# Kernel optimization log

Measured on AMD Instinct MI355X. Metric: run time of the kernel, lower is better.

## Reference

```python
import jax, jax.numpy as jnp
import numpy as np

INPUT_DIM = 1024
HIDDEN_DIM = 1024


def setup_inputs() -> dict:
    key = jax.random.key(0)
    ks = jax.random.split(key, 7)
    s = 1.0 / np.sqrt(INPUT_DIM)
    x = jax.random.normal(ks[0], (4, 2048, INPUT_DIM), dtype=jnp.float32)
    Wq = jax.random.uniform(ks[1], (INPUT_DIM, HIDDEN_DIM), minval=-s, maxval=s, dtype=jnp.float32)
    bq = jax.random.uniform(ks[2], (HIDDEN_DIM,), minval=-s, maxval=s, dtype=jnp.float32)
    Wk = jax.random.uniform(ks[3], (INPUT_DIM, HIDDEN_DIM), minval=-s, maxval=s, dtype=jnp.float32)
    bk = jax.random.uniform(ks[4], (HIDDEN_DIM,), minval=-s, maxval=s, dtype=jnp.float32)
    Wv = jax.random.uniform(ks[5], (INPUT_DIM, HIDDEN_DIM), minval=-s, maxval=s, dtype=jnp.float32)
    bv = jax.random.uniform(ks[6], (HIDDEN_DIM,), minval=-s, maxval=s, dtype=jnp.float32)
    return {"x": x, "Wq": Wq, "bq": bq, "Wk": Wk, "bk": bk, "Wv": Wv, "bv": bv}


def reference(x, Wq, bq, Wk, bk, Wv, bv):
    # Q, K, V: [B, S, H]
    Q = jnp.einsum('bsd,dh->bsh', x, Wq) + bq
    K = jnp.einsum('bsd,dh->bsh', x, Wk) + bk
    V = jnp.einsum('bsd,dh->bsh', x, Wv) + bv
    scale = 1.0 / jnp.sqrt(jnp.array(Q.shape[-1], dtype=Q.dtype))
    scores = jnp.einsum('bqh,bkh->bqk', Q, K) * scale  # [B, S, S]
    attn = jax.nn.softmax(scores, axis=-1)
    return jnp.einsum('bqk,bkh->bqh', attn, V)
```

## Files before the change

### kernel.cpp

```cpp
#include <hip/hip_runtime.h>
#include <hip/hip_bf16.h>
#include <stdint.h>

typedef unsigned short u16;
typedef __attribute__((ext_vector_type(8))) short short8;
typedef __attribute__((ext_vector_type(4))) float floatx4;

#define BATCH 4
#define SEQ   2048
#define DIM   1024

__device__ inline u16 f2bf(float f) {
  union { float f; uint32_t u; } v; v.f = f;
  uint32_t r = v.u + 0x7fffu + ((v.u >> 16) & 1u);
  return (u16)(r >> 16);
}

__device__ inline uint32_t f2bf2(float lo, float hi) {
  __hip_bfloat162 h = __float22bfloat162_rn(float2{lo, hi});
  union { __hip_bfloat162 h; uint32_t u; } v; v.h = h;
  return v.u;
}

__device__ inline void gload_lds16(const u16* g, u16* l) {
  __builtin_amdgcn_global_load_lds((const __attribute__((address_space(1))) uint32_t*)g,
                                   (__attribute__((address_space(3))) uint32_t*)l,
                                   16, 0, 0);
}

__global__ __launch_bounds__(256) void prep(const float* __restrict__ x,
                                            const float* __restrict__ Wq,
                                            const float* __restrict__ Wk,
                                            const float* __restrict__ Wv,
                                            const float* __restrict__ bq,
                                            const float* __restrict__ bk,
                                            const float* __restrict__ bv,
                                            u16* __restrict__ Xb,
                                            u16* __restrict__ Wt,
                                            float* __restrict__ bias,
                                            float* __restrict__ lsum) {
  __shared__ u16 tile[32][33];
  const int bx = blockIdx.x;
  if (bx < 8192) {
    size_t i = ((size_t)bx * 256 + threadIdx.x) * 4;
    float4 v = *(const float4*)(x + i);
    uint2 o;
    o.x = f2bf2(v.x, v.y);
    o.y = f2bf2(v.z, v.w);
    *(uint2*)(Xb + i) = o;
    if (bx < 8) {
      float4 z = {0.f, 0.f, 0.f, 0.f};
      *(float4*)(lsum + (size_t)bx * 1024 + threadIdx.x * 4) = z;
    }
    return;
  }
  const int t = bx - 8192;
  const int tz = t >> 10;
  const int bxx = t & 31;
  const int byy = (t >> 5) & 31;
  const float* W = (tz == 0) ? Wq : (tz == 1) ? Wk : Wv;
  u16* o = Wt + (size_t)tz * (1u << 20);
  if (bxx == 0 && byy == 0) {
    const float* bsrc = (tz == 0) ? bq : (tz == 1) ? bk : bv;
    float4 b4 = *(const float4*)(bsrc + threadIdx.x * 4);
    *(float4*)(bias + tz * 1024 + threadIdx.x * 4) = b4;
  }
  int c0 = bxx * 32, r0 = byy * 32;
  int tx = threadIdx.x & 31, ty = threadIdx.x >> 5;
#pragma unroll
  for (int p = 0; p < 4; ++p)
    tile[p * 8 + ty][tx] = f2bf(W[(size_t)(r0 + p * 8 + ty) * DIM + c0 + tx]);
  __syncthreads();
#pragma unroll
  for (int p = 0; p < 4; ++p)
    o[(size_t)(c0 + p * 8 + ty) * DIM + r0 + tx] = tile[tx][p * 8 + ty];
}


__global__ __launch_bounds__(256, 4)
void qkv_fused(const u16* __restrict__ Xb, const u16* __restrict__ Wt,
               u16* __restrict__ Q, u16* __restrict__ Vt,
               const float* __restrict__ bias) {
  constexpr int K = 1024;
  __shared__ u16 ldsA[128 * 64];
  __shared__ u16 ldsB[128 * 64];
  const int lane = threadIdx.x & 63;
  const int wave = threadIdx.x >> 6;
  const int z = blockIdx.z;

  int mt, nt, N;
  const u16 *Ab, *Bb;
  if (z < 2) {
    mt = blockIdx.x; nt = blockIdx.y; N = 1024;
    Ab = Xb + (size_t)mt * 128 * K;
    Bb = Wt + (size_t)z * (1u << 20) + (size_t)nt * 128 * K;
  } else {
    nt = blockIdx.x; mt = blockIdx.y; N = 8192;
    Ab = Wt + (size_t)2 * (1u << 20) + (size_t)mt * 128 * K;
    Bb = Xb + (size_t)nt * 128 * K;
  }

  const int sr = lane >> 2;
  const int sc = ((lane & 3) ^ ((lane >> 3) & 3)) * 8;
  const u16* gA0 = Ab + (size_t)(wave * 32 + sr) * K + sc;
  const u16* gB0 = Bb + (size_t)(wave * 32 + sr) * K + sc;
  u16* lA0 = ldsA + wave * 1024;
  u16* lB0 = ldsB + wave * 1024;
  constexpr int SL = 4096;

  const int wm = (wave >> 1) * 64;
  const int wn = (wave & 1) * 64;
  const int fr = lane & 15;
  const int fk = ((lane >> 4) ^ ((fr >> 1) & 3)) * 8;
  const u16* la = ldsA + (wm + fr) * 32 + fk;
  const u16* lb = ldsB + (wn + fr) * 32 + fk;

  floatx4 acc[4][4] = {};

  for (int kt = 0; kt < K; kt += 64) {
    __syncthreads();
#pragma unroll
    for (int i = 0; i < 2; ++i) {
      gload_lds16(gA0 + kt + (size_t)(16 * i) * K, lA0 + i * 512);
      gload_lds16(gA0 + kt + 32 + (size_t)(16 * i) * K, lA0 + SL + i * 512);
      gload_lds16(gB0 + kt + (size_t)(16 * i) * K, lB0 + i * 512);
      gload_lds16(gB0 + kt + 32 + (size_t)(16 * i) * K, lB0 + SL + i * 512);
    }
    __syncthreads();
#pragma unroll
    for (int ks = 0; ks < 2; ++ks) {
      short8 a[4], b[4];
#pragma unroll
      for (int i = 0; i < 4; ++i) a[i] = *(const short8*)(la + ks * SL + i * 512);
#pragma unroll
      for (int i = 0; i < 4; ++i) b[i] = *(const short8*)(lb + ks * SL + i * 512);
#pragma unroll
      for (int mi = 0; mi < 4; ++mi)
#pragma unroll
        for (int ni = 0; ni < 4; ++ni)
          acc[mi][ni] = __builtin_amdgcn_mfma_f32_16x16x32_bf16(a[mi], b[ni], acc[mi][ni], 0, 0, 0);
    }
  }

  const int er = (lane >> 4) * 4;
  const int ec = lane & 15;
  const int r0 = mt * 128 + wm;
  const int c0 = nt * 128 + wn;

  if (z < 2) {
    u16* C = Q + (size_t)z * (8u << 20);
    const float* bz = bias + z * 1024;
    const float zs = (z == 0) ? 0.03125f : 1.0f;
#pragma unroll
    for (int mi = 0; mi < 4; ++mi)
#pragma unroll
      for (int ni = 0; ni < 4; ++ni) {
        const int col = c0 + ni * 16 + ec;
        const float bb = bz[col];
        const int row = r0 + mi * 16 + er;
        const uint32_t p0 = f2bf2((acc[mi][ni][0] + bb) * zs, (acc[mi][ni][1] + bb) * zs);
        const uint32_t p1 = f2bf2((acc[mi][ni][2] + bb) * zs, (acc[mi][ni][3] + bb) * zs);
        C[(size_t)(row + 0) * N + col] = (u16)p0;
        C[(size_t)(row + 1) * N + col] = (u16)(p0 >> 16);
        C[(size_t)(row + 2) * N + col] = (u16)p1;
        C[(size_t)(row + 3) * N + col] = (u16)(p1 >> 16);
      }
  } else {
    const float* bz = bias + 2 * 1024;
#pragma unroll
    for (int mi = 0; mi < 4; ++mi) {
      float bb[4];
#pragma unroll
      for (int r = 0; r < 4; ++r) bb[r] = bz[r0 + mi * 16 + er + r];
#pragma unroll
      for (int ni = 0; ni < 4; ++ni) {
        const int col = c0 + ni * 16 + ec;
        const size_t base = (size_t)(col >> 11) * (1u << 21) + (col & 2047);
        const int row = r0 + mi * 16 + er;
        const uint32_t p0 = f2bf2(acc[mi][ni][0] + bb[0], acc[mi][ni][1] + bb[1]);
        const uint32_t p1 = f2bf2(acc[mi][ni][2] + bb[2], acc[mi][ni][3] + bb[3]);
        Vt[base + (size_t)(row + 0) * 2048] = (u16)p0;
        Vt[base + (size_t)(row + 1) * 2048] = (u16)(p0 >> 16);
        Vt[base + (size_t)(row + 2) * 2048] = (u16)p1;
        Vt[base + (size_t)(row + 3) * 2048] = (u16)(p1 >> 16);
      }
    }
  }
}

template <int EPI, int SWIZ, int TM>
__global__ __launch_bounds__(256, (TM == 256) ? 2 : 4)
void gemm_bt(const u16* __restrict__ A, const u16* __restrict__ Bt,
             void* __restrict__ Cv, float* __restrict__ lsum,
             int M, int N, int K, size_t sA, size_t sB, size_t sC) {
  constexpr int MI = TM / 32;
  constexpr int AS = TM / 64;
  __shared__ u16 ldsA[TM * 64];
  __shared__ u16 ldsB[128 * 64];
  const int lane = threadIdx.x & 63;
  const int wave = threadIdx.x >> 6;

  int mt, nt;
  if (SWIZ == 2) {
    const int lin = blockIdx.x;
    const int c = lin & 7, j = lin >> 3;
    mt = 4 * (c >> 1) + (j & 3);
    nt = 4 * (c & 1) + (j >> 2);
  } else {
    const int lin = blockIdx.x;
    const int c = lin & 7, j = lin >> 3;
    mt = 4 * (c & 1) + (j & 3);
    nt = 4 * (c >> 1) + (j >> 2);
  }

  const u16* Ab = A + sA * blockIdx.z + (size_t)mt * TM * K;
  const u16* Bb = Bt + sB * blockIdx.z + (size_t)nt * 128 * K;

  const int sr = lane >> 2;
  const int sc = ((lane & 3) ^ ((lane >> 3) & 3)) * 8;
  const u16* gA0 = Ab + (size_t)(wave * (TM / 4) + sr) * K + sc;
  const u16* gB0 = Bb + (size_t)(wave * 32 + sr) * K + sc;
  u16* lA0 = ldsA + wave * (TM / 4) * 32;
  u16* lB0 = ldsB + wave * 1024;
  constexpr int SLA = TM * 32;
  constexpr int SLB = 4096;

  const int wm = (wave >> 1) * (TM / 2);
  const int wn = (wave & 1) * 64;
  const int fr = lane & 15;
  const int fk = ((lane >> 4) ^ ((fr >> 1) & 3)) * 8;
  const u16* la = ldsA + (wm + fr) * 32 + fk;
  const u16* lb = ldsB + (wn + fr) * 32 + fk;

  floatx4 acc[MI][4] = {};

  for (int kt = 0; kt < K; kt += 64) {
    __syncthreads();
#pragma unroll
    for (int i = 0; i < AS; ++i) {
      gload_lds16(gA0 + kt + (size_t)(16 * i) * K, lA0 + i * 512);
      gload_lds16(gA0 + kt + 32 + (size_t)(16 * i) * K, lA0 + SLA + i * 512);
    }
#pragma unroll
    for (int i = 0; i < 2; ++i) {
      gload_lds16(gB0 + kt + (size_t)(16 * i) * K, lB0 + i * 512);
      gload_lds16(gB0 + kt + 32 + (size_t)(16 * i) * K, lB0 + SLB + i * 512);
    }
    __syncthreads();
#pragma unroll
    for (int ks = 0; ks < 2; ++ks) {
      short8 a[MI], b[4];
#pragma unroll
      for (int i = 0; i < MI; ++i)
        a[i] = *(const short8*)(la + ks * SLA + i * 512);
#pragma unroll
      for (int i = 0; i < 4; ++i)
        b[i] = *(const short8*)(lb + ks * SLB + i * 512);
#pragma unroll
      for (int mi = 0; mi < MI; ++mi)
#pragma unroll
        for (int ni = 0; ni < 4; ++ni)
          acc[mi][ni] = __builtin_amdgcn_mfma_f32_16x16x32_bf16(a[mi], b[ni], acc[mi][ni], 0, 0, 0);
    }
  }

  const int er = (lane >> 4) * 4;
  const int ec = lane & 15;
  const int r0 = mt * TM + wm;
  const int c0 = nt * 128 + wn;

  if (EPI == 1) {
    u16* C = (u16*)Cv + sC * blockIdx.z;
    float* lz = lsum + blockIdx.z * 2048;
#pragma unroll
    for (int mi = 0; mi < MI; ++mi) {
      float rs[4] = {0.f, 0.f, 0.f, 0.f};
#pragma unroll
      for (int ni = 0; ni < 4; ++ni) {
        const int col = c0 + ni * 16 + ec;
        const int row = r0 + mi * 16 + er;
        float e[4];
#pragma unroll
        for (int r = 0; r < 4; ++r) {
          e[r] = exp2f(acc[mi][ni][r] * 1.44269504088896340736f);
          rs[r] += e[r];
        }
        const uint32_t p0 = f2bf2(e[0], e[1]);
        const uint32_t p1 = f2bf2(e[2], e[3]);
        C[(size_t)(row + 0) * N + col] = (u16)p0;
        C[(size_t)(row + 1) * N + col] = (u16)(p0 >> 16);
        C[(size_t)(row + 2) * N + col] = (u16)p1;
        C[(size_t)(row + 3) * N + col] = (u16)(p1 >> 16);
      }
#pragma unroll
      for (int o = 1; o < 16; o <<= 1)
#pragma unroll
        for (int r = 0; r < 4; ++r) rs[r] += __shfl_xor(rs[r], o);
      if ((lane & 15) == 0) {
#pragma unroll
        for (int r = 0; r < 4; ++r)
          atomicAdd(&lz[r0 + mi * 16 + er + r], rs[r]);
      }
    }
  } else {
    float* C = (float*)Cv + sC * blockIdx.z;
    const float* lz = lsum + blockIdx.z * 2048;
#pragma unroll
    for (int mi = 0; mi < MI; ++mi) {
      float inv[4];
#pragma unroll
      for (int r = 0; r < 4; ++r) inv[r] = 1.0f / lz[r0 + mi * 16 + er + r];
#pragma unroll
      for (int ni = 0; ni < 4; ++ni) {
        const int col = c0 + ni * 16 + ec;
#pragma unroll
        for (int r = 0; r < 4; ++r) {
          const int row = r0 + mi * 16 + er + r;
          C[(size_t)row * N + col] = acc[mi][ni][r] * inv[r];
        }
      }
    }
  }
}

extern "C" void kernel_launch(void* const* d_in, const int* in_sizes, int n_in,
                              void* d_out, int out_size, void* d_ws, size_t ws_size,
                              hipStream_t stream) {
  const float* x  = (const float*)d_in[0];
  const float* Wq = (const float*)d_in[1];
  const float* bq = (const float*)d_in[2];
  const float* Wk = (const float*)d_in[3];
  const float* bk = (const float*)d_in[4];
  const float* Wv = (const float*)d_in[5];
  const float* bv = (const float*)d_in[6];
  float* out = (float*)d_out;

  char* ws = (char*)d_ws;
  const size_t MB = 1ull << 20;
  u16* Q    = (u16*)(ws + 0 * MB);
  u16* Kb   = (u16*)(ws + 16 * MB);
  u16* Vt   = (u16*)(ws + 48 * MB);
  u16* Xb   = (u16*)(ws + 64 * MB);
  u16* Wt   = (u16*)(ws + 80 * MB);
  float* bias = (float*)(ws + 86 * MB);
  float* lsum = (float*)(ws + 87 * MB);
  u16* P    = (u16*)(ws + 88 * MB);
  (void)Kb; (void)ws_size; (void)in_sizes; (void)n_in; (void)out_size;

  prep<<<11264, 256, 0, stream>>>(x, Wq, Wk, Wv, bq, bk, bv, Xb, Wt, bias, lsum);
  qkv_fused<<<dim3(64, 8, 3), 256, 0, stream>>>(Xb, Wt, Q, Vt, bias);
  gemm_bt<1, 4, 256><<<dim3(128, 1, 4), 256, 0, stream>>>(
      Q, Kb, P, lsum, 2048, 2048, 1024,
      (size_t)2097152, (size_t)2097152, (size_t)4194304);
  gemm_bt<2, 2, 128><<<dim3(128, 1, 4), 256, 0, stream>>>(
      P, Vt, out, lsum, 2048, 1024, 2048,
      (size_t)4194304, (size_t)2097152, (size_t)2097152);
}
```

Before: 232.7 us.

## Split PV GEMM over K with atomic accumulation and shrink score tiles

The PV GEMM is split into two halves along the key dimension, doubling its grid to 256 blocks per batch, and partial results are accumulated into the output with float atomicAdd. The output is zeroed by extra blocks in the prep kernel. The score GEMM moves from 256-row to 128-row tiles, also doubling its grid, and a shared k-loop helper replaces the templated GEMM. The aim is better CU occupancy on the MI355X's many CUs, at the cost of atomic traffic to the output and an extra zeroing pass.

```diff
diff --git a/kernel.cpp b/kernel.cpp
--- a/kernel.cpp
+++ b/kernel.cpp
@@ -38,7 +38,8 @@
                                             u16* __restrict__ Xb,
                                             u16* __restrict__ Wt,
                                             float* __restrict__ bias,
-                                            float* __restrict__ lsum) {
+                                            float* __restrict__ lsum,
+                                            float* __restrict__ out) {
   __shared__ u16 tile[32][33];
   const int bx = blockIdx.x;
   if (bx < 8192) {
@@ -54,6 +55,14 @@
     }
     return;
   }
+  if (bx >= 11264) {
+    const int b2 = bx - 11264;
+    const float4 z = {0.f, 0.f, 0.f, 0.f};
+#pragma unroll
+    for (int k = 0; k < 4; ++k)
+      *(float4*)(out + ((size_t)b2 * 1024 + k * 256 + threadIdx.x) * 4) = z;
+    return;
+  }
   const int t = bx - 8192;
   const int tz = t >> 10;
   const int bxx = t & 31;
@@ -77,11 +86,63 @@
 }
 
 
+template <int TM, int LD, int KLEN>
+__device__ __forceinline__ void kloop(const u16* __restrict__ Ab, const u16* __restrict__ Bb,
+                                      u16* __restrict__ ldsA, u16* __restrict__ ldsB,
+                                      int lane, int wave, floatx4 (&acc)[TM / 32][4]) {
+  constexpr int MI = TM / 32;
+  constexpr int AS = TM / 64;
+  const int sr = lane >> 2;
+  const int sc = ((lane & 3) ^ ((lane >> 3) & 3)) * 8;
+  const u16* gA0 = Ab + (size_t)(wave * (TM / 4) + sr) * LD + sc;
+  const u16* gB0 = Bb + (size_t)(wave * 32 + sr) * LD + sc;
+  u16* lA0 = ldsA + wave * (TM / 4) * 32;
+  u16* lB0 = ldsB + wave * 1024;
+  constexpr int SLA = TM * 32;
+  constexpr int SLB = 4096;
+
+  const int wm = (wave >> 1) * (TM / 2);
+  const int wn = (wave & 1) * 64;
+  const int fr = lane & 15;
+  const int fk = ((lane >> 4) ^ ((fr >> 1) & 3)) * 8;
+  const u16* la = ldsA + (wm + fr) * 32 + fk;
+  const u16* lb = ldsB + (wn + fr) * 32 + fk;
+
+  for (int kt = 0; kt < KLEN; kt += 64) {
+    __syncthreads();
+#pragma unroll
+    for (int i = 0; i < AS; ++i) {
+      gload_lds16(gA0 + kt + (size_t)(16 * i) * LD, lA0 + i * 512);
+      gload_lds16(gA0 + kt + 32 + (size_t)(16 * i) * LD, lA0 + SLA + i * 512);
+    }
+#pragma unroll
+    for (int i = 0; i < 2; ++i) {
+      gload_lds16(gB0 + kt + (size_t)(16 * i) * LD, lB0 + i * 512);
+      gload_lds16(gB0 + kt + 32 + (size_t)(16 * i) * LD, lB0 + SLB + i * 512);
+    }
+    __syncthreads();
+#pragma unroll
+    for (int ks = 0; ks < 2; ++ks) {
+      short8 a[MI], b[4];
+#pragma unroll
+      for (int i = 0; i < MI; ++i)
+        a[i] = *(const short8*)(la + ks * SLA + i * 512);
+#pragma unroll
+      for (int i = 0; i < 4; ++i)
+        b[i] = *(const short8*)(lb + ks * SLB + i * 512);
+#pragma unroll
+      for (int mi = 0; mi < MI; ++mi)
+#pragma unroll
+        for (int ni = 0; ni < 4; ++ni)
+          acc[mi][ni] = __builtin_amdgcn_mfma_f32_16x16x32_bf16(a[mi], b[ni], acc[mi][ni], 0, 0, 0);
+    }
+  }
+}
+
 __global__ __launch_bounds__(256, 4)
 void qkv_fused(const u16* __restrict__ Xb, const u16* __restrict__ Wt,
                u16* __restrict__ Q, u16* __restrict__ Vt,
                const float* __restrict__ bias) {
-  constexpr int K = 1024;
   __shared__ u16 ldsA[128 * 64];
   __shared__ u16 ldsB[128 * 64];
   const int lane = threadIdx.x & 63;
@@ -92,56 +153,19 @@
   const u16 *Ab, *Bb;
   if (z < 2) {
     mt = blockIdx.x; nt = blockIdx.y; N = 1024;
-    Ab = Xb + (size_t)mt * 128 * K;
-    Bb = Wt + (size_t)z * (1u << 20) + (size_t)nt * 128 * K;
+    Ab = Xb + (size_t)mt * 128 * 1024;
+    Bb = Wt + (size_t)z * (1u << 20) + (size_t)nt * 128 * 1024;
   } else {
     nt = blockIdx.x; mt = blockIdx.y; N = 8192;
-    Ab = Wt + (size_t)2 * (1u << 20) + (size_t)mt * 128 * K;
-    Bb = Xb + (size_t)nt * 128 * K;
-  }
-
-  const int sr = lane >> 2;
-  const int sc = ((lane & 3) ^ ((lane >> 3) & 3)) * 8;
-  const u16* gA0 = Ab + (size_t)(wave * 32 + sr) * K + sc;
-  const u16* gB0 = Bb + (size_t)(wave * 32 + sr) * K + sc;
-  u16* lA0 = ldsA + wave * 1024;
-  u16* lB0 = ldsB + wave * 1024;
-  constexpr int SL = 4096;
+    Ab = Wt + (size_t)2 * (1u << 20) + (size_t)mt * 128 * 1024;
+    Bb = Xb + (size_t)nt * 128 * 1024;
+  }
+
+  floatx4 acc[4][4] = {};
+  kloop<128, 1024, 1024>(Ab, Bb, ldsA, ldsB, lane, wave, acc);
 
   const int wm = (wave >> 1) * 64;
   const int wn = (wave & 1) * 64;
-  const int fr = lane & 15;
-  const int fk = ((lane >> 4) ^ ((fr >> 1) & 3)) * 8;
-  const u16* la = ldsA + (wm + fr) * 32 + fk;
-  const u16* lb = ldsB + (wn + fr) * 32 + fk;
-
-  floatx4 acc[4][4] = {};
-
-  for (int kt = 0; kt < K; kt += 64) {
-    __syncthreads();
-#pragma unroll
-    for (int i = 0; i < 2; ++i) {
-      gload_lds16(gA0 + kt + (size_t)(16 * i) * K, lA0 + i * 512);
-      gload_lds16(gA0 + kt + 32 + (size_t)(16 * i) * K, lA0 + SL + i * 512);
-      gload_lds16(gB0 + kt + (size_t)(16 * i) * K, lB0 + i * 512);
-      gload_lds16(gB0 + kt + 32 + (size_t)(16 * i) * K, lB0 + SL + i * 512);
-    }
-    __syncthreads();
-#pragma unroll
-    for (int ks = 0; ks < 2; ++ks) {
-      short8 a[4], b[4];
-#pragma unroll
-      for (int i = 0; i < 4; ++i) a[i] = *(const short8*)(la + ks * SL + i * 512);
-#pragma unroll
-      for (int i = 0; i < 4; ++i) b[i] = *(const short8*)(lb + ks * SL + i * 512);
-#pragma unroll
-      for (int mi = 0; mi < 4; ++mi)
-#pragma unroll
-        for (int ni = 0; ni < 4; ++ni)
-          acc[mi][ni] = __builtin_amdgcn_mfma_f32_16x16x32_bf16(a[mi], b[ni], acc[mi][ni], 0, 0, 0);
-    }
-  }
-
   const int er = (lane >> 4) * 4;
   const int ec = lane & 15;
   const int r0 = mt * 128 + wm;
@@ -188,136 +212,100 @@
   }
 }
 
-template <int EPI, int SWIZ, int TM>
-__global__ __launch_bounds__(256, (TM == 256) ? 2 : 4)
-void gemm_bt(const u16* __restrict__ A, const u16* __restrict__ Bt,
-             void* __restrict__ Cv, float* __restrict__ lsum,
-             int M, int N, int K, size_t sA, size_t sB, size_t sC) {
-  constexpr int MI = TM / 32;
-  constexpr int AS = TM / 64;
-  __shared__ u16 ldsA[TM * 64];
+__global__ __launch_bounds__(256, 4)
+void score_k(const u16* __restrict__ Q, u16* __restrict__ P, float* __restrict__ lsum) {
+  __shared__ u16 ldsA[128 * 64];
   __shared__ u16 ldsB[128 * 64];
   const int lane = threadIdx.x & 63;
   const int wave = threadIdx.x >> 6;
-
-  int mt, nt;
-  if (SWIZ == 2) {
-    const int lin = blockIdx.x;
-    const int c = lin & 7, j = lin >> 3;
-    mt = 4 * (c >> 1) + (j & 3);
-    nt = 4 * (c & 1) + (j >> 2);
-  } else {
-    const int lin = blockIdx.x;
-    const int c = lin & 7, j = lin >> 3;
-    mt = 4 * (c & 1) + (j & 3);
-    nt = 4 * (c >> 1) + (j >> 2);
-  }
-
-  const u16* Ab = A + sA * blockIdx.z + (size_t)mt * TM * K;
-  const u16* Bb = Bt + sB * blockIdx.z + (size_t)nt * 128 * K;
-
-  const int sr = lane >> 2;
-  const int sc = ((lane & 3) ^ ((lane >> 3) & 3)) * 8;
-  const u16* gA0 = Ab + (size_t)(wave * (TM / 4) + sr) * K + sc;
-  const u16* gB0 = Bb + (size_t)(wave * 32 + sr) * K + sc;
-  u16* lA0 = ldsA + wave * (TM / 4) * 32;
-  u16* lB0 = ldsB + wave * 1024;
-  constexpr int SLA = TM * 32;
-  constexpr int SLB = 4096;
-
-  const int wm = (wave >> 1) * (TM / 2);
+  const int z = blockIdx.z;
+  const int c = blockIdx.x & 7, j = blockIdx.x >> 3;
+  const int mt = 4 * (c >> 1) + (j & 3);
+  const int nt = 8 * (c & 1) + (j >> 2);
+  const u16* Ab = Q + (size_t)z * 2097152 + (size_t)mt * 128 * 1024;
+  const u16* Bb = Q + 8388608 + (size_t)z * 2097152 + (size_t)nt * 128 * 1024;
+
+  floatx4 acc[4][4] = {};
+  kloop<128, 1024, 1024>(Ab, Bb, ldsA, ldsB, lane, wave, acc);
+
+  const int wm = (wave >> 1) * 64;
   const int wn = (wave & 1) * 64;
-  const int fr = lane & 15;
-  const int fk = ((lane >> 4) ^ ((fr >> 1) & 3)) * 8;
-  const u16* la = ldsA + (wm + fr) * 32 + fk;
-  const u16* lb = ldsB + (wn + fr) * 32 + fk;
-
-  floatx4 acc[MI][4] = {};
-
-  for (int kt = 0; kt < K; kt += 64) {
-    __syncthreads();
-#pragma unroll
-    for (int i = 0; i < AS; ++i) {
-      gload_lds16(gA0 + kt + (size_t)(16 * i) * K, lA0 + i * 512);
-      gload_lds16(gA0 + kt + 32 + (size_t)(16 * i) * K, lA0 + SLA + i * 512);
-    }
-#pragma unroll
-    for (int i = 0; i < 2; ++i) {
-      gload_lds16(gB0 + kt + (size_t)(16 * i) * K, lB0 + i * 512);
-      gload_lds16(gB0 + kt + 32 + (size_t)(16 * i) * K, lB0 + SLB + i * 512);
-    }
-    __syncthreads();
-#pragma unroll
-    for (int ks = 0; ks < 2; ++ks) {
-      short8 a[MI], b[4];
-#pragma unroll
-      for (int i = 0; i < MI; ++i)
-        a[i] = *(const short8*)(la + ks * SLA + i * 512);
-#pragma unroll
-      for (int i = 0; i < 4; ++i)
-        b[i] = *(const short8*)(lb + ks * SLB + i * 512);
-#pragma unroll
-      for (int mi = 0; mi < MI; ++mi)
-#pragma unroll
-        for (int ni = 0; ni < 4; ++ni)
-          acc[mi][ni] = __builtin_amdgcn_mfma_f32_16x16x32_bf16(a[mi], b[ni], acc[mi][ni], 0, 0, 0);
-    }
-  }
-
   const int er = (lane >> 4) * 4;
   const int ec = lane & 15;
-  const int r0 = mt * TM + wm;
+  const int r0 = mt * 128 + wm;
   const int c0 = nt * 128 + wn;
-
-  if (EPI == 1) {
-    u16* C = (u16*)Cv + sC * blockIdx.z;
-    float* lz = lsum + blockIdx.z * 2048;
-#pragma unroll
-    for (int mi = 0; mi < MI; ++mi) {
-      float rs[4] = {0.f, 0.f, 0.f, 0.f};
-#pragma unroll
-      for (int ni = 0; ni < 4; ++ni) {
-        const int col = c0 + ni * 16 + ec;
-        const int row = r0 + mi * 16 + er;
-        float e[4];
-#pragma unroll
-        for (int r = 0; r < 4; ++r) {
-          e[r] = exp2f(acc[mi][ni][r] * 1.44269504088896340736f);
-          rs[r] += e[r];
-        }
-        const uint32_t p0 = f2bf2(e[0], e[1]);
-        const uint32_t p1 = f2bf2(e[2], e[3]);
-        C[(size_t)(row + 0) * N + col] = (u16)p0;
-        C[(size_t)(row + 1) * N + col] = (u16)(p0 >> 16);
-        C[(size_t)(row + 2) * N + col] = (u16)p1;
-        C[(size_t)(row + 3) * N + col] = (u16)(p1 >> 16);
+  u16* C = P + (size_t)z * 4194304;
+  float* lz = lsum + z * 2048;
+#pragma unroll
+  for (int mi = 0; mi < 4; ++mi) {
+    float rs[4] = {0.f, 0.f, 0.f, 0.f};
+#pragma unroll
+    for (int ni = 0; ni < 4; ++ni) {
+      const int col = c0 + ni * 16 + ec;
+      const int row = r0 + mi * 16 + er;
+      float e[4];
+#pragma unroll
+      for (int r = 0; r < 4; ++r) {
+        e[r] = exp2f(acc[mi][ni][r] * 1.44269504088896340736f);
+        rs[r] += e[r];
       }
-#pragma unroll
-      for (int o = 1; o < 16; o <<= 1)
-#pragma unroll
-        for (int r = 0; r < 4; ++r) rs[r] += __shfl_xor(rs[r], o);
-      if ((lane & 15) == 0) {
-#pragma unroll
-        for (int r = 0; r < 4; ++r)
-          atomicAdd(&lz[r0 + mi * 16 + er + r], rs[r]);
-      }
-    }
-  } else {
-    float* C = (float*)Cv + sC * blockIdx.z;
-    const float* lz = lsum + blockIdx.z * 2048;
-#pragma unroll
-    for (int mi = 0; mi < MI; ++mi) {
-      float inv[4];
-#pragma unroll
-      for (int r = 0; r < 4; ++r) inv[r] = 1.0f / lz[r0 + mi * 16 + er + r];
-#pragma unroll
-      for (int ni = 0; ni < 4; ++ni) {
-        const int col = c0 + ni * 16 + ec;
-#pragma unroll
-        for (int r = 0; r < 4; ++r) {
-          const int row = r0 + mi * 16 + er + r;
-          C[(size_t)row * N + col] = acc[mi][ni][r] * inv[r];
-        }
+      const uint32_t p0 = f2bf2(e[0], e[1]);
+      const uint32_t p1 = f2bf2(e[2], e[3]);
+      C[(size_t)(row + 0) * 2048 + col] = (u16)p0;
+      C[(size_t)(row + 1) * 2048 + col] = (u16)(p0 >> 16);
+      C[(size_t)(row + 2) * 2048 + col] = (u16)p1;
+      C[(size_t)(row + 3) * 2048 + col] = (u16)(p1 >> 16);
+    }
+#pragma unroll
+    for (int o = 1; o < 16; o <<= 1)
+#pragma unroll
+      for (int r = 0; r < 4; ++r) rs[r] += __shfl_xor(rs[r], o);
+    if ((lane & 15) == 0) {
+#pragma unroll
+      for (int r = 0; r < 4; ++r)
+        atomicAdd(&lz[r0 + mi * 16 + er + r], rs[r]);
+    }
+  }
+}
+
+__global__ __launch_bounds__(256, 4)
+void pv_k(const u16* __restrict__ P, const u16* __restrict__ Vt,
+          float* __restrict__ out, const float* __restrict__ lsum) {
+  __shared__ u16 ldsA[128 * 64];
+  __shared__ u16 ldsB[128 * 64];
+  const int lane = threadIdx.x & 63;
+  const int wave = threadIdx.x >> 6;
+  const int z = blockIdx.z;
+  const int c = blockIdx.x & 7, j = blockIdx.x >> 3;
+  const int mt = 4 * (c >> 1) + (j & 3);
+  const int nt = 4 * (c & 1) + ((j >> 2) & 3);
+  const int kh = j >> 4;
+  const u16* Ab = P + (size_t)z * 4194304 + (size_t)mt * 128 * 2048 + kh * 1024;
+  const u16* Bb = Vt + (size_t)z * 2097152 + (size_t)nt * 128 * 2048 + kh * 1024;
+
+  floatx4 acc[4][4] = {};
+  kloop<128, 2048, 1024>(Ab, Bb, ldsA, ldsB, lane, wave, acc);
+
+  const int wm = (wave >> 1) * 64;
+  const int wn = (wave & 1) * 64;
+  const int er = (lane >> 4) * 4;
+  const int ec = lane & 15;
+  const int r0 = mt * 128 + wm;
+  const int c0 = nt * 128 + wn;
+  float* C = out + (size_t)z * 2097152;
+  const float* lz = lsum + z * 2048;
+#pragma unroll
+  for (int mi = 0; mi < 4; ++mi) {
+    float inv[4];
+#pragma unroll
+    for (int r = 0; r < 4; ++r) inv[r] = 1.0f / lz[r0 + mi * 16 + er + r];
+#pragma unroll
+    for (int ni = 0; ni < 4; ++ni) {
+      const int col = c0 + ni * 16 + ec;
+#pragma unroll
+      for (int r = 0; r < 4; ++r) {
+        const int row = r0 + mi * 16 + er + r;
+        atomicAdd(&C[(size_t)row * 1024 + col], acc[mi][ni][r] * inv[r]);
       }
     }
   }
@@ -338,21 +326,16 @@
   char* ws = (char*)d_ws;
   const size_t MB = 1ull << 20;
   u16* Q    = (u16*)(ws + 0 * MB);
-  u16* Kb   = (u16*)(ws + 16 * MB);
   u16* Vt   = (u16*)(ws + 48 * MB);
   u16* Xb   = (u16*)(ws + 64 * MB);
   u16* Wt   = (u16*)(ws + 80 * MB);
   float* bias = (float*)(ws + 86 * MB);
   float* lsum = (float*)(ws + 87 * MB);
   u16* P    = (u16*)(ws + 88 * MB);
-  (void)Kb; (void)ws_size; (void)in_sizes; (void)n_in; (void)out_size;
-
-  prep<<<11264, 256, 0, stream>>>(x, Wq, Wk, Wv, bq, bk, bv, Xb, Wt, bias, lsum);
+  (void)ws_size; (void)in_sizes; (void)n_in; (void)out_size;
+
+  prep<<<13312, 256, 0, stream>>>(x, Wq, Wk, Wv, bq, bk, bv, Xb, Wt, bias, lsum, out);
   qkv_fused<<<dim3(64, 8, 3), 256, 0, stream>>>(Xb, Wt, Q, Vt, bias);
-  gemm_bt<1, 4, 256><<<dim3(128, 1, 4), 256, 0, stream>>>(
-      Q, Kb, P, lsum, 2048, 2048, 1024,
-      (size_t)2097152, (size_t)2097152, (size_t)4194304);
-  gemm_bt<2, 2, 128><<<dim3(128, 1, 4), 256, 0, stream>>>(
-      P, Vt, out, lsum, 2048, 1024, 2048,
-      (size_t)4194304, (size_t)2097152, (size_t)2097152);
-}
+  score_k<<<dim3(256, 1, 4), 256, 0, stream>>>(Q, P, lsum);
+  pv_k<<<dim3(256, 1, 4), 256, 0, stream>>>(P, Vt, out, lsum);
+}
```

New measurement: 273.9 us. 17.7% more time.
